# Optimization experiments

Hardware: AMD Instinct MI355X
Metric: run time of the kernel (lower is better)

Reference implementation:

```python
import jax, jax.numpy as jnp
import numpy as np

N, CIN, COUT, H, CH, K, M = 60000, 128, 128, 8, 16, 27, 960000


def setup_inputs() -> dict:
    key = jax.random.key(0)
    ks = jax.random.split(key, 12)
    f32 = jnp.float32
    s = 1.0 / np.sqrt(CIN)
    return {
        "feats": jax.random.normal(ks[0], (N, CIN), f32),
        "norm_points": jax.random.uniform(ks[1], (N, 3), f32) - 0.5,
        "w1": jax.random.normal(ks[2], (3, 3), f32) * 0.5,
        "bn1_scale": jnp.ones((3,), f32),
        "bn1_shift": jnp.zeros((3,), f32),
        "w2": jax.random.normal(ks[3], (3, CIN), f32) * 0.5,
        "bn2_scale": jnp.ones((CIN,), f32),
        "bn2_shift": jnp.zeros((CIN,), f32),
        "w3": jax.random.normal(ks[4], (CIN, CIN), f32) * s,
        "b3": jnp.zeros((CIN,), f32),
        "wq": jax.random.normal(ks[5], (CIN, COUT), f32) * s,
        "bq": jnp.zeros((COUT,), f32),
        "wv": jax.random.normal(ks[6], (CIN, COUT), f32) * s,
        "bv": jnp.zeros((COUT,), f32),
        "wo": jax.random.normal(ks[7], (COUT, COUT), f32) * s,
        "bo": jnp.zeros((COUT,), f32),
        "pos_enc": jax.random.normal(ks[8], (K, H, CH), f32),
        # kq_map row0 = key_idx * K + kernel_offset; row1 = query_idx
        "kq_row0": jax.random.randint(ks[9], (M,), 0, N * K, dtype=jnp.int32).astype(jnp.int64),
        "kq_row1": jax.random.randint(ks[10], (M,), 0, N, dtype=jnp.int32).astype(jnp.int64),
    }


def _l2norm(x):
    # F.normalize(p=2, dim=-1) with eps clamp
    n = jnp.linalg.norm(x, axis=-1, keepdims=True)
    return x / jnp.maximum(n, 1e-12)


def reference(feats, norm_points, w1, bn1_scale, bn1_shift, w2, bn2_scale, bn2_shift,
              w3, b3, wq, bq, wv, bv, wo, bo, pos_enc, kq_row0, kq_row1):
    # intra-voxel positional MLP (BN folded to eval-mode scale/shift)
    h = jax.nn.relu((norm_points @ w1) * bn1_scale + bn1_shift)
    h = jax.nn.relu((h @ w2) * bn2_scale + bn2_shift)
    x = feats + (h @ w3 + b3)                      # [N, CIN]

    q = (x @ wq + bq).reshape(N, H, CH)            # [N, H, CH]
    v = (x @ wv + bv).reshape(N, H, CH)

    nq = _l2norm(q)                                # normalized queries
    npos = _l2norm(pos_enc)                        # [K, H, CH]

    koff = kq_row0 % K                             # kernel-offset index into pos_enc
    kidx = kq_row0 // K                            # key (value) index

    # dot_product_cuda: attn[m,h] = <nq[query_m], npos[offset_m]>
    attn = jnp.einsum('mhc,mhc->mh', nq[kq_row1], npos[koff])   # [M, H]

    # scalar_attention_cuda: out[query_m] += attn[m] * v[key_m]
    msg = attn[:, :, None] * v[kidx]                             # [M, H, CH]
    out = jax.ops.segment_sum(msg, kq_row1, num_segments=N)      # [N, H, CH]

    return out.reshape(N, COUT) @ wo + bo
```

## Files before the change

### kernel.cpp

```cpp
#include <hip/hip_runtime.h>
#include <hip/hip_bf16.h>

#define NPTS  60000
#define KK    27
#define NEDGE 960000
#define CAP   96

__global__ __launch_bounds__(256) void tiny_mlp_kernel(
    const float* __restrict__ npnts,
    const float* __restrict__ w1, const float* __restrict__ bn1s, const float* __restrict__ bn1h,
    const float* __restrict__ w2, const float* __restrict__ bn2s, const float* __restrict__ bn2h,
    float* __restrict__ h2out) {
    __shared__ float w2s[3 * 128];
    __shared__ float sc2[128], sh2[128];
    __shared__ float w1s[9], sc1[3], sh1[3];
    __shared__ float h2s[64 * 129];

    const int tid = threadIdx.x;
    for (int i = tid; i < 384; i += 256) w2s[i] = w2[i];
    if (tid < 128) { sc2[tid] = bn2s[tid]; sh2[tid] = bn2h[tid]; }
    if (tid < 9) w1s[tid] = w1[tid];
    if (tid < 3) { sc1[tid] = bn1s[tid]; sh1[tid] = bn1h[tid]; }
    __syncthreads();

    const int p  = tid >> 2;
    const int cq = (tid & 3) * 32;
    const int pt = blockIdx.x * 64 + p;
    float h1a = 0.f, h1b = 0.f, h1c = 0.f;
    if (pt < NPTS) {
        float p0 = npnts[pt * 3 + 0], p1 = npnts[pt * 3 + 1], p2 = npnts[pt * 3 + 2];
        float t0 = p0 * w1s[0] + p1 * w1s[3] + p2 * w1s[6];
        float t1 = p0 * w1s[1] + p1 * w1s[4] + p2 * w1s[7];
        float t2 = p0 * w1s[2] + p1 * w1s[5] + p2 * w1s[8];
        h1a = fmaxf(t0 * sc1[0] + sh1[0], 0.f);
        h1b = fmaxf(t1 * sc1[1] + sh1[1], 0.f);
        h1c = fmaxf(t2 * sc1[2] + sh1[2], 0.f);
    }
    for (int c = cq; c < cq + 32; ++c) {
        float t = h1a * w2s[c] + h1b * w2s[128 + c] + h1c * w2s[256 + c];
        h2s[p * 129 + c] = fmaxf(t * sc2[c] + sh2[c], 0.f);
    }
    __syncthreads();
    for (int i = tid; i < 64 * 128; i += 256) {
        int row = i >> 7, col = i & 127;
        int gr = blockIdx.x * 64 + row;
        if (gr < NPTS) h2out[gr * 128 + col] = h2s[row * 129 + col];
    }
}

template <int MODE>
__global__ __launch_bounds__(256, 4) void gemm128_kernel(
    const float* __restrict__ in, const float* __restrict__ w,
    const float* __restrict__ bias, const float* __restrict__ resid,
    float* __restrict__ out) {
    __shared__ float xs[128][36];
    __shared__ float ws[32][132];
    const int tid = threadIdx.x;
    const int rb  = blockIdx.x * 128;
    const int tr  = tid >> 4;
    const int tc  = tid & 15;
    const int c0  = tc * 8;

    float acc[8][8];
#pragma unroll
    for (int i = 0; i < 8; ++i)
#pragma unroll
        for (int j = 0; j < 8; ++j) acc[i][j] = 0.f;

    const int srow  = tid >> 3;
    const int skq   = (tid & 7) * 4;
    const int wkrow = tid >> 5;
    const int wcq   = (tid & 31) * 4;

    for (int k0 = 0; k0 < 128; k0 += 32) {
        __syncthreads();
#pragma unroll
        for (int rr = 0; rr < 128; rr += 32) {
            int gr = rb + srow + rr;
            float4 val = make_float4(0.f, 0.f, 0.f, 0.f);
            if (gr < NPTS) val = *(const float4*)&in[gr * 128 + k0 + skq];
            *(float4*)&xs[srow + rr][skq] = val;
        }
#pragma unroll
        for (int kk = 0; kk < 32; kk += 8)
            *(float4*)&ws[wkrow + kk][wcq] = *(const float4*)&w[(k0 + wkrow + kk) * 128 + wcq];
        __syncthreads();
#pragma unroll 2
        for (int k = 0; k < 32; ++k) {
            float4 b0 = *(float4*)&ws[k][c0];
            float4 b1 = *(float4*)&ws[k][c0 + 4];
            float av[8];
#pragma unroll
            for (int i = 0; i < 8; ++i) av[i] = xs[tr + 16 * i][k];
#pragma unroll
            for (int i = 0; i < 8; ++i) {
                acc[i][0] = fmaf(av[i], b0.x, acc[i][0]);
                acc[i][1] = fmaf(av[i], b0.y, acc[i][1]);
                acc[i][2] = fmaf(av[i], b0.z, acc[i][2]);
                acc[i][3] = fmaf(av[i], b0.w, acc[i][3]);
                acc[i][4] = fmaf(av[i], b1.x, acc[i][4]);
                acc[i][5] = fmaf(av[i], b1.y, acc[i][5]);
                acc[i][6] = fmaf(av[i], b1.z, acc[i][6]);
                acc[i][7] = fmaf(av[i], b1.w, acc[i][7]);
            }
        }
    }

    float breg[8];
#pragma unroll
    for (int j = 0; j < 8; ++j) breg[j] = bias[c0 + j];

#pragma unroll
    for (int i = 0; i < 8; ++i) {
        int gr = rb + tr + 16 * i;
        float o[8];
#pragma unroll
        for (int j = 0; j < 8; ++j) o[j] = acc[i][j] + breg[j];
        if (MODE == 1) {
            if (gr < NPTS) {
                float4 f0 = *(const float4*)&resid[gr * 128 + c0];
                float4 f1 = *(const float4*)&resid[gr * 128 + c0 + 4];
                o[0] += f0.x; o[1] += f0.y; o[2] += f0.z; o[3] += f0.w;
                o[4] += f1.x; o[5] += f1.y; o[6] += f1.z; o[7] += f1.w;
            }
        }
        if (MODE == 2) {
            float ss = 0.f;
#pragma unroll
            for (int j = 0; j < 8; ++j) ss += o[j] * o[j];
            ss += __shfl_xor(ss, 1);
            float inv = 1.f / fmaxf(sqrtf(ss), 1e-12f);
#pragma unroll
            for (int j = 0; j < 8; ++j) o[j] *= inv;
        }
        if (gr < NPTS) {
            float4* op = (float4*)&out[gr * 128 + c0];
            op[0] = make_float4(o[0], o[1], o[2], o[3]);
            op[1] = make_float4(o[4], o[5], o[6], o[7]);
        }
    }
}

__global__ __launch_bounds__(256) void zero_cnt_kernel(int* __restrict__ cnt) {
    int i = blockIdx.x * 256 + threadIdx.x;
    if (i < NPTS) cnt[i] = 0;
}

__global__ __launch_bounds__(256) void build_buckets_kernel(
    const int* __restrict__ r0, const int* __restrict__ r1,
    int* __restrict__ cnt, int* __restrict__ bucket) {
    int m = blockIdx.x * 256 + threadIdx.x;
    if (m >= NEDGE) return;
    int a = r0[m];
    int q = r1[m];
    if (q < 0 || q >= NPTS) return;
    if (a < 0 || a >= NPTS * KK) return;
    int kidx = a / KK;
    int koff = a - kidx * KK;
    int slot = atomicAdd(&cnt[q], 1);
    if (slot < CAP) bucket[q * CAP + slot] = (kidx << 5) | koff;
}

__global__ __launch_bounds__(256, 8) void attn_scatter_kernel(
    const float* __restrict__ nq, const float* __restrict__ v,
    const float* __restrict__ pos_enc, const int* __restrict__ cnt,
    const int* __restrict__ bucket, float* __restrict__ pre) {
    __shared__ float nps[KK * 128];

    const int tid = threadIdx.x;
    if (tid < KK * 8) {
        const float4* pv = (const float4*)&pos_enc[tid * 16];
        float4 a = pv[0], b = pv[1], c = pv[2], d = pv[3];
        float ss = a.x*a.x + a.y*a.y + a.z*a.z + a.w*a.w
                 + b.x*b.x + b.y*b.y + b.z*b.z + b.w*b.w
                 + c.x*c.x + c.y*c.y + c.z*c.z + c.w*c.w
                 + d.x*d.x + d.y*d.y + d.z*d.z + d.w*d.w;
        float inv = 1.f / fmaxf(sqrtf(ss), 1e-12f);
        float4* o = (float4*)&nps[tid * 16];
        o[0] = make_float4(a.x*inv, a.y*inv, a.z*inv, a.w*inv);
        o[1] = make_float4(b.x*inv, b.y*inv, b.z*inv, b.w*inv);
        o[2] = make_float4(c.x*inv, c.y*inv, c.z*inv, c.w*inv);
        o[3] = make_float4(d.x*inv, d.y*inv, d.z*inv, d.w*inv);
    }
    __syncthreads();

    const int l = tid & 63;
    const int wid = blockIdx.x * 4 + (tid >> 6);
    const int nwaves = gridDim.x * 4;

#define ATT_EDGE(REC) do {                                                  \
        int koff_ = (REC) & 31; int kidx_ = (REC) >> 5;                     \
        float2 np_ = *(const float2*)&nps[koff_ * 128 + 2 * l];             \
        float2 v_  = *(const float2*)&v[kidx_ * 128 + 2 * l];               \
        float a_ = nq2.x * np_.x + nq2.y * np_.y;                           \
        a_ += __shfl_xor(a_, 1); a_ += __shfl_xor(a_, 2);                   \
        a_ += __shfl_xor(a_, 4);                                            \
        accx = fmaf(a_, v_.x, accx); accy = fmaf(a_, v_.y, accy);           \
    } while (0)

    for (int n = wid; n < NPTS; n += nwaves) {
        float2 nq2 = *(const float2*)&nq[n * 128 + 2 * l];
        int deg = min(cnt[n], CAP);
        int base = n * CAP;
        int myrec = (l < deg) ? bucket[base + l] : 0;
        float accx = 0.f, accy = 0.f;
        int dmain = min(deg, 64);
        int e = 0;
        for (; e + 4 <= dmain; e += 4) {
            int r0 = __shfl(myrec, e);
            int r1 = __shfl(myrec, e + 1);
            int r2 = __shfl(myrec, e + 2);
            int r3 = __shfl(myrec, e + 3);
            ATT_EDGE(r0); ATT_EDGE(r1); ATT_EDGE(r2); ATT_EDGE(r3);
        }
        for (; e < dmain; ++e) {
            int r = __shfl(myrec, e);
            ATT_EDGE(r);
        }
        for (; e < deg; ++e) {
            int r = bucket[base + e];
            ATT_EDGE(r);
        }
        *(float2*)&pre[n * 128 + 2 * l] = make_float2(accx, accy);
    }
#undef ATT_EDGE
}

extern "C" void kernel_launch(void* const* d_in, const int* in_sizes, int n_in,
                              void* d_out, int out_size, void* d_ws, size_t ws_size,
                              hipStream_t stream) {
    const float* feats = (const float*)d_in[0];
    const float* npnts = (const float*)d_in[1];
    const float* w1    = (const float*)d_in[2];
    const float* bn1s  = (const float*)d_in[3];
    const float* bn1h  = (const float*)d_in[4];
    const float* w2    = (const float*)d_in[5];
    const float* bn2s  = (const float*)d_in[6];
    const float* bn2h  = (const float*)d_in[7];
    const float* w3    = (const float*)d_in[8];
    const float* b3    = (const float*)d_in[9];
    const float* wq    = (const float*)d_in[10];
    const float* bq    = (const float*)d_in[11];
    const float* wv    = (const float*)d_in[12];
    const float* bv    = (const float*)d_in[13];
    const float* wo    = (const float*)d_in[14];
    const float* bo    = (const float*)d_in[15];
    const float* pos   = (const float*)d_in[16];
    const int*   r0    = (const int*)d_in[17];
    const int*   r1    = (const int*)d_in[18];
    float* out = (float*)d_out;

    float* h2buf = (float*)d_ws;
    float* xbuf  = h2buf + (size_t)NPTS * 128;
    float* nqbuf = xbuf  + (size_t)NPTS * 128;
    float* vbuf  = nqbuf + (size_t)NPTS * 128;
    float* prebuf = xbuf;
    int*   cnt    = (int*)h2buf;
    int*   bucket = cnt + NPTS;

    dim3 blk(256);
    const int nb64  = (NPTS + 63) / 64;
    const int nb128 = (NPTS + 127) / 128;

    tiny_mlp_kernel<<<nb64, blk, 0, stream>>>(npnts, w1, bn1s, bn1h, w2, bn2s, bn2h, h2buf);
    gemm128_kernel<1><<<nb128, blk, 0, stream>>>(h2buf, w3, b3, feats, xbuf);
    gemm128_kernel<2><<<nb128, blk, 0, stream>>>(xbuf, wq, bq, nullptr, nqbuf);
    gemm128_kernel<0><<<nb128, blk, 0, stream>>>(xbuf, wv, bv, nullptr, vbuf);
    zero_cnt_kernel<<<(NPTS + 255) / 256, blk, 0, stream>>>(cnt);
    build_buckets_kernel<<<(NEDGE + 255) / 256, blk, 0, stream>>>(r0, r1, cnt, bucket);
    attn_scatter_kernel<<<2048, blk, 0, stream>>>(nqbuf, vbuf, pos, cnt, bucket, prebuf);
    gemm128_kernel<0><<<nb128, blk, 0, stream>>>(prebuf, wo, bo, nullptr, out);
}
```

Before: 381.4 us.

## Replace FP32 SIMT GEMMs with split-bf16 MFMA GEMMs

Replaces the four 128x128 FP32 register-tiled GEMMs with a matrix-core kernel using bf16 MFMA 16x16x32. Precision is kept near FP32 by splitting each operand into hi and lo bf16 parts and issuing three MFMAs per tile. Each block converts the full weight matrix into hi/lo bf16 layouts in LDS, and A fragments are loaded directly from global memory. This removes SIMT FMA cost but adds per-block weight conversion and narrower scalar output stores.

```diff
diff --git a/kernel.cpp b/kernel.cpp
--- a/kernel.cpp
+++ b/kernel.cpp
@@ -5,6 +5,14 @@
 #define KK    27
 #define NEDGE 960000
 #define CAP   96
+
+typedef __attribute__((ext_vector_type(8))) short bf16x8;
+typedef __attribute__((ext_vector_type(4))) float f32x4;
+
+__device__ __forceinline__ unsigned short f2bf(float x) {
+    unsigned u = __float_as_uint(x);
+    return (unsigned short)((u + 0x7FFFu + ((u >> 16) & 1u)) >> 16);
+}
 
 __global__ __launch_bounds__(256) void tiny_mlp_kernel(
     const float* __restrict__ npnts,
@@ -49,94 +57,97 @@
 }
 
 template <int MODE>
-__global__ __launch_bounds__(256, 4) void gemm128_kernel(
+__global__ __launch_bounds__(256, 2) void mfma_gemm_kernel(
     const float* __restrict__ in, const float* __restrict__ w,
     const float* __restrict__ bias, const float* __restrict__ resid,
     float* __restrict__ out) {
-    __shared__ float xs[128][36];
-    __shared__ float ws[32][132];
+    __shared__ short whi[16384];
+    __shared__ short wlo[16384];
     const int tid = threadIdx.x;
-    const int rb  = blockIdx.x * 128;
-    const int tr  = tid >> 4;
-    const int tc  = tid & 15;
-    const int c0  = tc * 8;
-
-    float acc[8][8];
-#pragma unroll
-    for (int i = 0; i < 8; ++i)
-#pragma unroll
-        for (int j = 0; j < 8; ++j) acc[i][j] = 0.f;
-
-    const int srow  = tid >> 3;
-    const int skq   = (tid & 7) * 4;
-    const int wkrow = tid >> 5;
-    const int wcq   = (tid & 31) * 4;
-
-    for (int k0 = 0; k0 < 128; k0 += 32) {
-        __syncthreads();
-#pragma unroll
-        for (int rr = 0; rr < 128; rr += 32) {
-            int gr = rb + srow + rr;
-            float4 val = make_float4(0.f, 0.f, 0.f, 0.f);
-            if (gr < NPTS) val = *(const float4*)&in[gr * 128 + k0 + skq];
-            *(float4*)&xs[srow + rr][skq] = val;
-        }
-#pragma unroll
-        for (int kk = 0; kk < 32; kk += 8)
-            *(float4*)&ws[wkrow + kk][wcq] = *(const float4*)&w[(k0 + wkrow + kk) * 128 + wcq];
-        __syncthreads();
-#pragma unroll 2
-        for (int k = 0; k < 32; ++k) {
-            float4 b0 = *(float4*)&ws[k][c0];
-            float4 b1 = *(float4*)&ws[k][c0 + 4];
-            float av[8];
-#pragma unroll
-            for (int i = 0; i < 8; ++i) av[i] = xs[tr + 16 * i][k];
-#pragma unroll
-            for (int i = 0; i < 8; ++i) {
-                acc[i][0] = fmaf(av[i], b0.x, acc[i][0]);
-                acc[i][1] = fmaf(av[i], b0.y, acc[i][1]);
-                acc[i][2] = fmaf(av[i], b0.z, acc[i][2]);
-                acc[i][3] = fmaf(av[i], b0.w, acc[i][3]);
-                acc[i][4] = fmaf(av[i], b1.x, acc[i][4]);
-                acc[i][5] = fmaf(av[i], b1.y, acc[i][5]);
-                acc[i][6] = fmaf(av[i], b1.z, acc[i][6]);
-                acc[i][7] = fmaf(av[i], b1.w, acc[i][7]);
+
+    {
+        const float4* w4 = (const float4*)w;
+#pragma unroll
+        for (int it = 0; it < 16; ++it) {
+            int i4 = tid + 256 * it;
+            int k  = i4 >> 5;
+            int c0 = (i4 & 31) * 4;
+            float4 val = w4[i4];
+            float vv[4] = {val.x, val.y, val.z, val.w};
+            int ks  = k >> 5;
+            int kin = k & 31;
+            int q   = kin >> 3;
+            int s   = kin & 7;
+#pragma unroll
+            for (int j = 0; j < 4; ++j) {
+                int c   = c0 + j;
+                int t   = c >> 4;
+                int c16 = c & 15;
+                int idx = ((((ks * 8 + t) * 4 + q) * 16 + c16) << 3) | s;
+                unsigned short h = f2bf(vv[j]);
+                float hf = __uint_as_float((unsigned)h << 16);
+                unsigned short l = f2bf(vv[j] - hf);
+                whi[idx] = (short)h;
+                wlo[idx] = (short)l;
             }
         }
     }
-
-    float breg[8];
-#pragma unroll
-    for (int j = 0; j < 8; ++j) breg[j] = bias[c0 + j];
-
-#pragma unroll
-    for (int i = 0; i < 8; ++i) {
-        int gr = rb + tr + 16 * i;
-        float o[8];
-#pragma unroll
-        for (int j = 0; j < 8; ++j) o[j] = acc[i][j] + breg[j];
-        if (MODE == 1) {
-            if (gr < NPTS) {
-                float4 f0 = *(const float4*)&resid[gr * 128 + c0];
-                float4 f1 = *(const float4*)&resid[gr * 128 + c0 + 4];
-                o[0] += f0.x; o[1] += f0.y; o[2] += f0.z; o[3] += f0.w;
-                o[4] += f1.x; o[5] += f1.y; o[6] += f1.z; o[7] += f1.w;
+    __syncthreads();
+
+    const int lane = tid & 63;
+    const int wv   = tid >> 6;
+    const int q    = lane >> 4;
+    const int cl   = lane & 15;
+    const int row0 = blockIdx.x * 64 + wv * 16;
+    const int arow = min(row0 + cl, NPTS - 1);
+
+    f32x4 acc[8];
+#pragma unroll
+    for (int t = 0; t < 8; ++t) acc[t] = (f32x4){0.f, 0.f, 0.f, 0.f};
+
+#pragma unroll
+    for (int ks = 0; ks < 4; ++ks) {
+        const float4 c1 = *(const float4*)&in[arow * 128 + ks * 32 + q * 8];
+        const float4 c2 = *(const float4*)&in[arow * 128 + ks * 32 + q * 8 + 4];
+        float av[8] = {c1.x, c1.y, c1.z, c1.w, c2.x, c2.y, c2.z, c2.w};
+        bf16x8 ah, al;
+#pragma unroll
+        for (int j = 0; j < 8; ++j) {
+            unsigned short h = f2bf(av[j]);
+            float hf = __uint_as_float((unsigned)h << 16);
+            ah[j] = (short)h;
+            al[j] = (short)f2bf(av[j] - hf);
+        }
+#pragma unroll
+        for (int t = 0; t < 8; ++t) {
+            const int cb = ((((ks * 8 + t) * 4 + q) * 16 + cl) << 3);
+            bf16x8 bh = *(const bf16x8*)&whi[cb];
+            bf16x8 bl = *(const bf16x8*)&wlo[cb];
+            acc[t] = __builtin_amdgcn_mfma_f32_16x16x32_bf16(ah, bh, acc[t], 0, 0, 0);
+            acc[t] = __builtin_amdgcn_mfma_f32_16x16x32_bf16(al, bh, acc[t], 0, 0, 0);
+            acc[t] = __builtin_amdgcn_mfma_f32_16x16x32_bf16(ah, bl, acc[t], 0, 0, 0);
+        }
+    }
+
+#pragma unroll
+    for (int t = 0; t < 8; ++t) {
+        float bv_ = bias[t * 16 + cl];
+#pragma unroll
+        for (int r = 0; r < 4; ++r) {
+            int row = row0 + q * 4 + r;
+            float o = acc[t][r] + bv_;
+            if (MODE == 1) {
+                if (row < NPTS) o += resid[row * 128 + t * 16 + cl];
             }
-        }
-        if (MODE == 2) {
-            float ss = 0.f;
-#pragma unroll
-            for (int j = 0; j < 8; ++j) ss += o[j] * o[j];
-            ss += __shfl_xor(ss, 1);
-            float inv = 1.f / fmaxf(sqrtf(ss), 1e-12f);
-#pragma unroll
-            for (int j = 0; j < 8; ++j) o[j] *= inv;
-        }
-        if (gr < NPTS) {
-            float4* op = (float4*)&out[gr * 128 + c0];
-            op[0] = make_float4(o[0], o[1], o[2], o[3]);
-            op[1] = make_float4(o[4], o[5], o[6], o[7]);
+            if (MODE == 2) {
+                float ss = o * o;
+                ss += __shfl_xor(ss, 1);
+                ss += __shfl_xor(ss, 2);
+                ss += __shfl_xor(ss, 4);
+                ss += __shfl_xor(ss, 8);
+                o *= 1.f / fmaxf(sqrtf(ss), 1e-12f);
+            }
+            if (row < NPTS) out[row * 128 + t * 16 + cl] = o;
         }
     }
 }
@@ -259,15 +270,14 @@
     int*   bucket = cnt + NPTS;
 
     dim3 blk(256);
-    const int nb64  = (NPTS + 63) / 64;
-    const int nb128 = (NPTS + 127) / 128;
+    const int nb64 = (NPTS + 63) / 64;
 
     tiny_mlp_kernel<<<nb64, blk, 0, stream>>>(npnts, w1, bn1s, bn1h, w2, bn2s, bn2h, h2buf);
-    gemm128_kernel<1><<<nb128, blk, 0, stream>>>(h2buf, w3, b3, feats, xbuf);
-    gemm128_kernel<2><<<nb128, blk, 0, stream>>>(xbuf, wq, bq, nullptr, nqbuf);
-    gemm128_kernel<0><<<nb128, blk, 0, stream>>>(xbuf, wv, bv, nullptr, vbuf);
+    mfma_gemm_kernel<1><<<nb64, blk, 0, stream>>>(h2buf, w3, b3, feats, xbuf);
+    mfma_gemm_kernel<2><<<nb64, blk, 0, stream>>>(xbuf, wq, bq, nullptr, nqbuf);
+    mfma_gemm_kernel<0><<<nb64, blk, 0, stream>>>(xbuf, wv, bv, nullptr, vbuf);
     zero_cnt_kernel<<<(NPTS + 255) / 256, blk, 0, stream>>>(cnt);
     build_buckets_kernel<<<(NEDGE + 255) / 256, blk, 0, stream>>>(r0, r1, cnt, bucket);
     attn_scatter_kernel<<<2048, blk, 0, stream>>>(nqbuf, vbuf, pos, cnt, bucket, prebuf);
-    gemm128_kernel<0><<<nb128, blk, 0, stream>>>(prebuf, wo, bo, nullptr, out);
-}
+    mfma_gemm_kernel<0><<<nb64, blk, 0, stream>>>(prebuf, wo, bo, nullptr, out);
+}
```

After: 445.7 us. 1.17x slower.
